# Optimization experiments

Hardware: AMD Instinct MI355X
Metric: run time of the kernel (lower is better)

The kernel has to match this reference:

```python
import jax, jax.numpy as jnp
import numpy as np

N_HEADS = 16


def setup_inputs() -> dict:
    key = jax.random.key(0)
    ks = jax.random.split(key, 9)
    B, S, D = 2, 2048, 1024
    sc = 0.02
    return {
        'x': jax.random.normal(ks[0], (B, S, D), jnp.float32),
        'Wq': jax.random.normal(ks[1], (D, D), jnp.float32) * sc,
        'bq': jax.random.normal(ks[2], (D,), jnp.float32) * sc,
        'Wk': jax.random.normal(ks[3], (D, D), jnp.float32) * sc,
        'bk': jax.random.normal(ks[4], (D,), jnp.float32) * sc,
        'Wv': jax.random.normal(ks[5], (D, D), jnp.float32) * sc,
        'bv': jax.random.normal(ks[6], (D,), jnp.float32) * sc,
        'Wo': jax.random.normal(ks[7], (D, D), jnp.float32) * sc,
        'bo': jax.random.normal(ks[8], (D,), jnp.float32) * sc,
    }


def reference(x, Wq, bq, Wk, bk, Wv, bv, Wo, bo):
    # Chunked causal prefill. The chunk-wise mask (q_pos >= kv_pos over the
    # growing KV cache) is mathematically identical to full causal attention,
    # so we compute it as one vectorized masked softmax attention.
    B, S, D = x.shape
    H = N_HEADS
    hd = D // H

    def proj(W, b):
        # torch Linear: y = x @ W.T + b ; then split heads -> [B,H,S,hd]
        y = jnp.einsum('bsd,ed->bse', x, W) + b
        return y.reshape(B, S, H, hd).transpose(0, 2, 1, 3)

    q = proj(Wq, bq)
    k = proj(Wk, bk)
    v = proj(Wv, bv)

    scores = jnp.einsum('bhqd,bhkd->bhqk', q, k) / jnp.sqrt(jnp.asarray(hd, x.dtype))
    causal = jnp.tril(jnp.ones((S, S), dtype=bool))  # [S,S]
    scores = jnp.where(causal[None, None], scores, jnp.asarray(-jnp.inf, scores.dtype))
    attn = jax.nn.softmax(scores, axis=-1)
    ctx = jnp.einsum('bhqk,bhkd->bhqd', attn, v)  # [B,H,S,hd]
    ctx = ctx.transpose(0, 2, 1, 3).reshape(B, S, D)
    out = jnp.einsum('bsd,ed->bse', ctx, Wo) + bo
    return out
```

## Files before the change

kernel.cpp:

```cpp
#include <hip/hip_runtime.h>
#include <cstdint>
#include <math.h>

typedef _Float16 f16;
typedef _Float16 f16x2 __attribute__((ext_vector_type(2)));
typedef _Float16 f16x4 __attribute__((ext_vector_type(4)));
typedef _Float16 f16x8 __attribute__((ext_vector_type(8)));
typedef __fp16   h16x2 __attribute__((ext_vector_type(2)));
typedef float    f32x4 __attribute__((ext_vector_type(4)));

__device__ __forceinline__ f32x4 mfma16(f16x8 a, f16x8 b, f32x4 c) {
  return __builtin_amdgcn_mfma_f32_16x16x32_f16(a, b, c, 0, 0, 0);
}
__device__ __forceinline__ void gl2lds16(const f16* g, f16* l) {
  __builtin_amdgcn_global_load_lds((__attribute__((address_space(1))) void*)(g),
                                   (__attribute__((address_space(3))) void*)(l),
                                   16, 0, 0);
}
__device__ __forceinline__ float fexp2(float x) { return __builtin_amdgcn_exp2f(x); }
__device__ __forceinline__ f16x2 pkrtz(float a, float b) {
  h16x2 r = __builtin_amdgcn_cvt_pkrtz(a, b);
  return __builtin_bit_cast(f16x2, r);
}
__device__ __forceinline__ float dot2acc(f16x2 a, f16x2 b, float c) {
#if __has_builtin(__builtin_amdgcn_fdot2)
  return __builtin_amdgcn_fdot2(__builtin_bit_cast(h16x2, a),
                                __builtin_bit_cast(h16x2, b), c, false);
#else
  return c + (float)a[0] * (float)b[0] + (float)a[1] * (float)b[1];
#endif
}

__global__ __launch_bounds__(256) void cvt_kernel(
    const float* __restrict__ x,  const float* __restrict__ wq, const float* __restrict__ wk,
    const float* __restrict__ wv, const float* __restrict__ wo,
    f16* __restrict__ xh, f16* __restrict__ wqkvh, f16* __restrict__ woh)
{
  const int seg = blockIdx.y;
  const float* src; f16* dst; int n;
  if      (seg == 0) { src = x;  dst = xh;              n = 4194304; }
  else if (seg == 1) { src = wq; dst = wqkvh;           n = 1048576; }
  else if (seg == 2) { src = wk; dst = wqkvh + 1048576; n = 1048576; }
  else if (seg == 3) { src = wv; dst = wqkvh + 2097152; n = 1048576; }
  else               { src = wo; dst = woh;             n = 1048576; }
  const int idx = (int)(blockIdx.x * 256 + threadIdx.x) * 8;
  if (idx >= n) return;
  f32x4 a = *(const f32x4*)(src + idx);
  f32x4 b = *(const f32x4*)(src + idx + 4);
  f16x8 h;
  h[0] = (f16)a[0]; h[1] = (f16)a[1]; h[2] = (f16)a[2]; h[3] = (f16)a[3];
  h[4] = (f16)b[0]; h[5] = (f16)b[1]; h[6] = (f16)b[2]; h[7] = (f16)b[3];
  *(f16x8*)(dst + idx) = h;
}

__global__ __launch_bounds__(256) void gemm_qkv(
    const f16* __restrict__ A, const f16* __restrict__ B,
    const float* __restrict__ bias0, const float* __restrict__ bias1, const float* __restrict__ bias2,
    f16* __restrict__ Qp, f16* __restrict__ Kp, f16* __restrict__ Vtp)
{
  constexpr int K = 1024;
  __shared__ __align__(16) f16 As[128 * 32];
  __shared__ __align__(16) f16 Bs[128 * 32];
  const int tid  = threadIdx.x;
  const int wave = tid >> 6, lane = tid & 63;
  const int quad = lane >> 4, col = lane & 15;
  const int tile_m = blockIdx.y * 128, tile_n = blockIdx.x * 128;
  const int mb = (wave >> 1) * 64, nb = (wave & 1) * 64;
  const int srow = lane >> 2, scol = (lane & 3) * 8;
  const f16* gA = A + (size_t)(tile_m + wave * 32 + srow) * K + scol;
  const f16* gB = B + (size_t)(tile_n + wave * 32 + srow) * K + scol;
  f16* lA = As + wave * 1024;
  f16* lB = Bs + wave * 1024;

  f32x4 acc[4][4] = {};
  for (int k0 = 0; k0 < K; k0 += 32) {
    gl2lds16(gA + k0,          lA);
    gl2lds16(gA + 16 * K + k0, lA + 512);
    gl2lds16(gB + k0,          lB);
    gl2lds16(gB + 16 * K + k0, lB + 512);
    __syncthreads();
    f16x8 af[4], bf[4];
    #pragma unroll
    for (int i = 0; i < 4; ++i)
      af[i] = *(const f16x8*)&As[(mb + i * 16 + col) * 32 + quad * 8];
    #pragma unroll
    for (int j = 0; j < 4; ++j)
      bf[j] = *(const f16x8*)&Bs[(nb + j * 16 + col) * 32 + quad * 8];
    #pragma unroll
    for (int i = 0; i < 4; ++i)
      #pragma unroll
      for (int j = 0; j < 4; ++j)
        acc[i][j] = mfma16(af[i], bf[j], acc[i][j]);
    __syncthreads();
  }

  #pragma unroll
  for (int j = 0; j < 4; ++j) {
    const int gn = tile_n + nb + j * 16 + col;
    const int which = gn >> 10;
    const int d = gn & 1023;
    const int h = d >> 6, hi = d & 63;
    if (which == 2) {
      const float bvv = bias2[d];
      #pragma unroll
      for (int i = 0; i < 4; ++i) {
        const int gm0 = tile_m + mb + i * 16 + quad * 4;
        const int bb = gm0 >> 11, s = gm0 & 2047;
        f16x4 pw;
        #pragma unroll
        for (int r = 0; r < 4; ++r) pw[r] = (f16)(acc[i][j][r] + bvv);
        *(f16x4*)&Vtp[(((size_t)bb * 16 + h) * 64 + hi) * 2048 + s] = pw;
      }
    } else {
      const float* bp = (which == 0) ? bias0 : bias1;
      f16* dst        = (which == 0) ? Qp    : Kp;
      const float bvv = bp[d];
      const float qs  = (which == 0) ? 0.18033688f : 1.0f;
      #pragma unroll
      for (int i = 0; i < 4; ++i) {
        #pragma unroll
        for (int r = 0; r < 4; ++r) {
          const int gm = tile_m + mb + i * 16 + quad * 4 + r;
          const int bb = gm >> 11, s = gm & 2047;
          dst[(((size_t)bb * 16 + h) * 2048 + s) * 64 + hi] = (f16)((acc[i][j][r] + bvv) * qs);
        }
      }
    }
  }
}

__global__ __launch_bounds__(128) void attn_kernel(
    const f16* __restrict__ Q, const f16* __restrict__ K, const f16* __restrict__ Vt,
    f16* __restrict__ ctx)
{
  __shared__ __align__(16) f16 Ks[64 * 72];
  __shared__ __align__(16) f16 Vts[64 * 72];
  __shared__ __align__(16) f16 Ps[2][32 * 72];
  __shared__ __align__(16) float abuf[2][32];
  __shared__ __align__(16) float lbuf[2][32];

  const int bh  = blockIdx.x;
  const int by  = blockIdx.y;
  const int qt  = (by < 16) ? by : 47 - by;
  const int tid = threadIdx.x;
  const int wave = tid >> 6, lane = tid & 63;
  const int quad = lane >> 4, col = lane & 15;
  const int b = bh >> 4, h = bh & 15;
  const size_t base = (size_t)bh * 2048 * 64;
  const size_t vtb  = (size_t)bh * 64 * 2048;

  int srow[4], sc8[4];
  #pragma unroll
  for (int i = 0; i < 4; ++i) {
    const int flat = tid + i * 128;
    srow[i] = flat >> 3;
    sc8[i]  = (flat & 7) * 8;
  }

  const int q0 = qt * 64;
  const int qa = q0 + wave * 16;
  const int qb = q0 + 32 + wave * 16;
  const f16x8 bqa0 = *(const f16x8*)&Q[base + (size_t)(qa + col) * 64 + quad * 8];
  const f16x8 bqa1 = *(const f16x8*)&Q[base + (size_t)(qa + col) * 64 + 32 + quad * 8];
  const f16x8 bqb0 = *(const f16x8*)&Q[base + (size_t)(qb + col) * 64 + quad * 8];
  const f16x8 bqb1 = *(const f16x8*)&Q[base + (size_t)(qb + col) * 64 + 32 + quad * 8];

  f32x4 cta[4] = {}, ctb[4] = {};
  float ma = -INFINITY, la = 0.f, mb = -INFINITY, lb = 0.f;

  f16x8 kr[4], vr[4];
  auto gload = [&](int t) {
    #pragma unroll
    for (int i = 0; i < 4; ++i) {
      kr[i] = *(const f16x8*)&K[base + (size_t)(t * 64 + srow[i]) * 64 + sc8[i]];
      vr[i] = *(const f16x8*)&Vt[vtb + (size_t)srow[i] * 2048 + t * 64 + sc8[i]];
    }
  };
  gload(0);

  const int nIter = qt + 1;
  for (int t = 0; t < nIter; ++t) {
    __syncthreads();
    #pragma unroll
    for (int i = 0; i < 4; ++i) {
      *(f16x8*)&Ks[srow[i] * 72 + sc8[i]]  = kr[i];
      *(f16x8*)&Vts[srow[i] * 72 + sc8[i]] = vr[i];
    }
    __syncthreads();
    if (t + 1 < nIter) gload(t + 1);

    f32x4 sa[4], sb[4];
    #pragma unroll
    for (int jt = 0; jt < 4; ++jt) {
      const int kro = (jt * 16 + col) * 72;
      const f16x8 ak0 = *(const f16x8*)&Ks[kro + quad * 8];
      const f16x8 ak1 = *(const f16x8*)&Ks[kro + 32 + quad * 8];
      f32x4 za = {}, zb = {};
      za = mfma16(ak0, bqa0, za); sa[jt] = mfma16(ak1, bqa1, za);
      zb = mfma16(ak0, bqb0, zb); sb[jt] = mfma16(ak1, bqb1, zb);
    }

    if (t == qt) {
      #pragma unroll
      for (int jt = 0; jt < 4; ++jt) {
        const int kg = t * 64 + jt * 16 + quad * 4;
        #pragma unroll
        for (int r = 0; r < 4; ++r) {
          if (kg + r > qa + col) sa[jt][r] = -1e30f;
          if (kg + r > qb + col) sb[jt][r] = -1e30f;
        }
      }
    }

    const f16x2 one2 = {(_Float16)1.f, (_Float16)1.f};
    {
      float tm = fmaxf(fmaxf(sa[0][0], sa[0][1]), fmaxf(sa[0][2], sa[0][3]));
      #pragma unroll
      for (int jt = 1; jt < 4; ++jt)
        tm = fmaxf(tm, fmaxf(fmaxf(sa[jt][0], sa[jt][1]), fmaxf(sa[jt][2], sa[jt][3])));
      tm = fmaxf(tm, __shfl_xor(tm, 16));
      tm = fmaxf(tm, __shfl_xor(tm, 32));
      const float mnew = fmaxf(ma, tm);
      const float alpha = fexp2(ma - mnew);
      ma = mnew;
      float rs = 0.f;
      #pragma unroll
      for (int jt = 0; jt < 4; ++jt) {
        const f16x2 a01 = pkrtz(fexp2(sa[jt][0] - mnew), fexp2(sa[jt][1] - mnew));
        const f16x2 a23 = pkrtz(fexp2(sa[jt][2] - mnew), fexp2(sa[jt][3] - mnew));
        rs = dot2acc(a01, one2, rs);
        rs = dot2acc(a23, one2, rs);
        f16x4 pw; pw[0] = a01[0]; pw[1] = a01[1]; pw[2] = a23[0]; pw[3] = a23[1];
        *(f16x4*)&Ps[wave][col * 72 + jt * 16 + quad * 4] = pw;
      }
      rs += __shfl_xor(rs, 16);
      rs += __shfl_xor(rs, 32);
      la = la * alpha + rs;
      if (quad == 0) abuf[wave][col] = alpha;
    }
    {
      float tm = fmaxf(fmaxf(sb[0][0], sb[0][1]), fmaxf(sb[0][2], sb[0][3]));
      #pragma unroll
      for (int jt = 1; jt < 4; ++jt)
        tm = fmaxf(tm, fmaxf(fmaxf(sb[jt][0], sb[jt][1]), fmaxf(sb[jt][2], sb[jt][3])));
      tm = fmaxf(tm, __shfl_xor(tm, 16));
      tm = fmaxf(tm, __shfl_xor(tm, 32));
      const float mnew = fmaxf(mb, tm);
      const float alpha = fexp2(mb - mnew);
      mb = mnew;
      float rs = 0.f;
      #pragma unroll
      for (int jt = 0; jt < 4; ++jt) {
        const f16x2 a01 = pkrtz(fexp2(sb[jt][0] - mnew), fexp2(sb[jt][1] - mnew));
        const f16x2 a23 = pkrtz(fexp2(sb[jt][2] - mnew), fexp2(sb[jt][3] - mnew));
        rs = dot2acc(a01, one2, rs);
        rs = dot2acc(a23, one2, rs);
        f16x4 pw; pw[0] = a01[0]; pw[1] = a01[1]; pw[2] = a23[0]; pw[3] = a23[1];
        *(f16x4*)&Ps[wave][(16 + col) * 72 + jt * 16 + quad * 4] = pw;
      }
      rs += __shfl_xor(rs, 16);
      rs += __shfl_xor(rs, 32);
      lb = lb * alpha + rs;
      if (quad == 0) abuf[wave][16 + col] = alpha;
    }

    __asm__ volatile("s_waitcnt lgkmcnt(0)" ::: "memory");
    const f32x4 ava = *(const f32x4*)&abuf[wave][quad * 4];
    const f32x4 avb = *(const f32x4*)&abuf[wave][16 + quad * 4];
    #pragma unroll
    for (int jd = 0; jd < 4; ++jd) { cta[jd] *= ava; ctb[jd] *= avb; }

    const f16x8 apa0 = *(const f16x8*)&Ps[wave][col * 72 + quad * 8];
    const f16x8 apa1 = *(const f16x8*)&Ps[wave][col * 72 + 32 + quad * 8];
    const f16x8 apb0 = *(const f16x8*)&Ps[wave][(16 + col) * 72 + quad * 8];
    const f16x8 apb1 = *(const f16x8*)&Ps[wave][(16 + col) * 72 + 32 + quad * 8];
    #pragma unroll
    for (int jd = 0; jd < 4; ++jd) {
      const int vro = (jd * 16 + col) * 72;
      const f16x8 bv0 = *(const f16x8*)&Vts[vro + quad * 8];
      const f16x8 bv1 = *(const f16x8*)&Vts[vro + 32 + quad * 8];
      cta[jd] = mfma16(apa1, bv1, mfma16(apa0, bv0, cta[jd]));
      ctb[jd] = mfma16(apb1, bv1, mfma16(apb0, bv0, ctb[jd]));
    }
  }

  if (quad == 0) { lbuf[wave][col] = la; lbuf[wave][16 + col] = lb; }
  __asm__ volatile("s_waitcnt lgkmcnt(0)" ::: "memory");
  const f32x4 lva = *(const f32x4*)&lbuf[wave][quad * 4];
  const f32x4 lvb = *(const f32x4*)&lbuf[wave][16 + quad * 4];
  #pragma unroll
  for (int jd = 0; jd < 4; ++jd) {
    #pragma unroll
    for (int r = 0; r < 4; ++r) {
      const int qga = qa + quad * 4 + r;
      const int qgb = qb + quad * 4 + r;
      const int d = h * 64 + jd * 16 + col;
      ctx[((size_t)b * 2048 + qga) * 1024 + d] = (f16)(cta[jd][r] / lva[r]);
      ctx[((size_t)b * 2048 + qgb) * 1024 + d] = (f16)(ctb[jd][r] / lvb[r]);
    }
  }
}

__global__ __launch_bounds__(256) void gemm_o(
    const f16* __restrict__ A, const f16* __restrict__ B, const float* __restrict__ bias,
    float* __restrict__ Out)
{
  constexpr int K = 1024;
  __shared__ __align__(16) f16 As[128 * 32];
  __shared__ __align__(16) f16 Bs[64 * 32];
  const int tid  = threadIdx.x;
  const int wave = tid >> 6, lane = tid & 63;
  const int quad = lane >> 4, col = lane & 15;
  const int tile_m = blockIdx.y * 128, tile_n = blockIdx.x * 64;
  const int mb = wave * 32;
  const int srow = lane >> 2, scol = (lane & 3) * 8;
  const f16* gA = A + (size_t)(tile_m + wave * 32 + srow) * K + scol;
  const f16* gB = B + (size_t)(tile_n + wave * 16 + srow) * K + scol;
  f16* lA = As + wave * 1024;
  f16* lB = Bs + wave * 512;

  f32x4 acc[2][4] = {};
  for (int k0 = 0; k0 < K; k0 += 32) {
    gl2lds16(gA + k0,          lA);
    gl2lds16(gA + 16 * K + k0, lA + 512);
    gl2lds16(gB + k0,          lB);
    __syncthreads();
    f16x8 af[2], bf[4];
    #pragma unroll
    for (int i = 0; i < 2; ++i)
      af[i] = *(const f16x8*)&As[(mb + i * 16 + col) * 32 + quad * 8];
    #pragma unroll
    for (int j = 0; j < 4; ++j)
      bf[j] = *(const f16x8*)&Bs[(j * 16 + col) * 32 + quad * 8];
    #pragma unroll
    for (int i = 0; i < 2; ++i)
      #pragma unroll
      for (int j = 0; j < 4; ++j)
        acc[i][j] = mfma16(af[i], bf[j], acc[i][j]);
    __syncthreads();
  }

  #pragma unroll
  for (int j = 0; j < 4; ++j) {
    const int gn = tile_n + j * 16 + col;
    const float bvv = bias[gn];
    #pragma unroll
    for (int i = 0; i < 2; ++i) {
      #pragma unroll
      for (int r = 0; r < 4; ++r) {
        const int gm = tile_m + mb + i * 16 + quad * 4 + r;
        Out[(size_t)gm * 1024 + gn] = acc[i][j][r] + bvv;
      }
    }
  }
}

extern "C" void kernel_launch(void* const* d_in, const int* in_sizes, int n_in,
                              void* d_out, int out_size, void* d_ws, size_t ws_size,
                              hipStream_t stream)
{
  const float* x  = (const float*)d_in[0];
  const float* Wq = (const float*)d_in[1];
  const float* bq = (const float*)d_in[2];
  const float* Wk = (const float*)d_in[3];
  const float* bk = (const float*)d_in[4];
  const float* Wv = (const float*)d_in[5];
  const float* bv = (const float*)d_in[6];
  const float* Wo = (const float*)d_in[7];
  const float* bo = (const float*)d_in[8];
  float* out = (float*)d_out;

  f16* ws = (f16*)d_ws;
  const size_t M1 = 1048576;
  f16* xh    = ws;
  f16* wqkvh = ws + 4  * M1;
  f16* woh   = ws + 7  * M1;
  f16* Qh    = ws + 8  * M1;
  f16* Kh    = ws + 12 * M1;
  f16* Vth   = ws + 16 * M1;
  f16* ctxh  = ws + 20 * M1;

  cvt_kernel<<<dim3(2048, 5), 256, 0, stream>>>(x, Wq, Wk, Wv, Wo, xh, wqkvh, woh);
  gemm_qkv<<<dim3(24, 32), 256, 0, stream>>>(xh, wqkvh, bq, bk, bv, Qh, Kh, Vth);
  attn_kernel<<<dim3(32, 32), 128, 0, stream>>>(Qh, Kh, Vth, ctxh);
  gemm_o<<<dim3(16, 32), 256, 0, stream>>>(ctxh, woh, bo, out);
}
```

Baseline: 214.2 us.

## Restructure attention to single-wave blocks loading K/V straight from global memory

The attention kernel now runs one 64-thread wave per block, each handling 32 query rows, on a 32x64 grid scheduled longest-causal-work first. K and V^T fragments are read directly from global memory into registers, which removes the LDS staging buffers and both __syncthreads per tile. The alpha and row-sum broadcasts move from LDS to lane shuffles. In exchange, K/V tiles are no longer shared between waves, so L2 traffic doubles, and global loads are no longer prefetched a tile ahead, which exposes load latency unless occupancy hides it.

```diff
diff --git a/kernel.cpp b/kernel.cpp
--- a/kernel.cpp
+++ b/kernel.cpp
@@ -129,37 +129,23 @@
   }
 }
 
-__global__ __launch_bounds__(128) void attn_kernel(
+__global__ __launch_bounds__(64, 2) void attn_kernel(
     const f16* __restrict__ Q, const f16* __restrict__ K, const f16* __restrict__ Vt,
     f16* __restrict__ ctx)
 {
-  __shared__ __align__(16) f16 Ks[64 * 72];
-  __shared__ __align__(16) f16 Vts[64 * 72];
-  __shared__ __align__(16) f16 Ps[2][32 * 72];
-  __shared__ __align__(16) float abuf[2][32];
-  __shared__ __align__(16) float lbuf[2][32];
-
-  const int bh  = blockIdx.x;
-  const int by  = blockIdx.y;
-  const int qt  = (by < 16) ? by : 47 - by;
-  const int tid = threadIdx.x;
-  const int wave = tid >> 6, lane = tid & 63;
+  __shared__ __align__(16) f16 Ps[32 * 72];
+
+  const int bh   = blockIdx.x;
+  const int slot = 63 - (int)blockIdx.y;
+  const int lane = threadIdx.x;
   const int quad = lane >> 4, col = lane & 15;
   const int b = bh >> 4, h = bh & 15;
   const size_t base = (size_t)bh * 2048 * 64;
   const size_t vtb  = (size_t)bh * 64 * 2048;
 
-  int srow[4], sc8[4];
-  #pragma unroll
-  for (int i = 0; i < 4; ++i) {
-    const int flat = tid + i * 128;
-    srow[i] = flat >> 3;
-    sc8[i]  = (flat & 7) * 8;
-  }
-
-  const int q0 = qt * 64;
-  const int qa = q0 + wave * 16;
-  const int qb = q0 + 32 + wave * 16;
+  const int q0 = slot * 32;
+  const int qa = q0, qb = q0 + 16;
+
   const f16x8 bqa0 = *(const f16x8*)&Q[base + (size_t)(qa + col) * 64 + quad * 8];
   const f16x8 bqa1 = *(const f16x8*)&Q[base + (size_t)(qa + col) * 64 + 32 + quad * 8];
   const f16x8 bqb0 = *(const f16x8*)&Q[base + (size_t)(qb + col) * 64 + quad * 8];
@@ -168,39 +154,34 @@
   f32x4 cta[4] = {}, ctb[4] = {};
   float ma = -INFINITY, la = 0.f, mb = -INFINITY, lb = 0.f;
 
-  f16x8 kr[4], vr[4];
-  auto gload = [&](int t) {
-    #pragma unroll
-    for (int i = 0; i < 4; ++i) {
-      kr[i] = *(const f16x8*)&K[base + (size_t)(t * 64 + srow[i]) * 64 + sc8[i]];
-      vr[i] = *(const f16x8*)&Vt[vtb + (size_t)srow[i] * 2048 + t * 64 + sc8[i]];
-    }
-  };
-  gload(0);
-
-  const int nIter = qt + 1;
+  const f16* kf = K  + base + (size_t)col * 64 + quad * 8;
+  const f16* vf = Vt + vtb  + (size_t)col * 2048 + quad * 8;
+
+  const int nIter = (slot >> 1) + 1;
   for (int t = 0; t < nIter; ++t) {
-    __syncthreads();
-    #pragma unroll
-    for (int i = 0; i < 4; ++i) {
-      *(f16x8*)&Ks[srow[i] * 72 + sc8[i]]  = kr[i];
-      *(f16x8*)&Vts[srow[i] * 72 + sc8[i]] = vr[i];
-    }
-    __syncthreads();
-    if (t + 1 < nIter) gload(t + 1);
+    f16x8 ak0[4], ak1[4], bv0[4], bv1[4];
+    const f16* kt = kf + (size_t)t * 4096;
+    const f16* vt = vf + t * 64;
+    #pragma unroll
+    for (int j = 0; j < 4; ++j) {
+      ak0[j] = *(const f16x8*)&kt[(size_t)j * 1024];
+      ak1[j] = *(const f16x8*)&kt[(size_t)j * 1024 + 32];
+    }
+    #pragma unroll
+    for (int j = 0; j < 4; ++j) {
+      bv0[j] = *(const f16x8*)&vt[(size_t)j * 32768];
+      bv1[j] = *(const f16x8*)&vt[(size_t)j * 32768 + 32];
+    }
 
     f32x4 sa[4], sb[4];
     #pragma unroll
     for (int jt = 0; jt < 4; ++jt) {
-      const int kro = (jt * 16 + col) * 72;
-      const f16x8 ak0 = *(const f16x8*)&Ks[kro + quad * 8];
-      const f16x8 ak1 = *(const f16x8*)&Ks[kro + 32 + quad * 8];
       f32x4 za = {}, zb = {};
-      za = mfma16(ak0, bqa0, za); sa[jt] = mfma16(ak1, bqa1, za);
-      zb = mfma16(ak0, bqb0, zb); sb[jt] = mfma16(ak1, bqb1, zb);
-    }
-
-    if (t == qt) {
+      za = mfma16(ak0[jt], bqa0, za); sa[jt] = mfma16(ak1[jt], bqa1, za);
+      zb = mfma16(ak0[jt], bqb0, zb); sb[jt] = mfma16(ak1[jt], bqb1, zb);
+    }
+
+    if (t == nIter - 1) {
       #pragma unroll
       for (int jt = 0; jt < 4; ++jt) {
         const int kg = t * 64 + jt * 16 + quad * 4;
@@ -213,6 +194,7 @@
     }
 
     const f16x2 one2 = {(_Float16)1.f, (_Float16)1.f};
+    f32x4 ava, avb;
     {
       float tm = fmaxf(fmaxf(sa[0][0], sa[0][1]), fmaxf(sa[0][2], sa[0][3]));
       #pragma unroll
@@ -231,12 +213,13 @@
         rs = dot2acc(a01, one2, rs);
         rs = dot2acc(a23, one2, rs);
         f16x4 pw; pw[0] = a01[0]; pw[1] = a01[1]; pw[2] = a23[0]; pw[3] = a23[1];
-        *(f16x4*)&Ps[wave][col * 72 + jt * 16 + quad * 4] = pw;
+        *(f16x4*)&Ps[col * 72 + jt * 16 + quad * 4] = pw;
       }
       rs += __shfl_xor(rs, 16);
       rs += __shfl_xor(rs, 32);
       la = la * alpha + rs;
-      if (quad == 0) abuf[wave][col] = alpha;
+      #pragma unroll
+      for (int r = 0; r < 4; ++r) ava[r] = __shfl(alpha, quad * 4 + r);
     }
     {
       float tm = fmaxf(fmaxf(sb[0][0], sb[0][1]), fmaxf(sb[0][2], sb[0][3]));
@@ -256,38 +239,37 @@
         rs = dot2acc(a01, one2, rs);
         rs = dot2acc(a23, one2, rs);
         f16x4 pw; pw[0] = a01[0]; pw[1] = a01[1]; pw[2] = a23[0]; pw[3] = a23[1];
-        *(f16x4*)&Ps[wave][(16 + col) * 72 + jt * 16 + quad * 4] = pw;
+        *(f16x4*)&Ps[(16 + col) * 72 + jt * 16 + quad * 4] = pw;
       }
       rs += __shfl_xor(rs, 16);
       rs += __shfl_xor(rs, 32);
       lb = lb * alpha + rs;
-      if (quad == 0) abuf[wave][16 + col] = alpha;
-    }
+      #pragma unroll
+      for (int r = 0; r < 4; ++r) avb[r] = __shfl(alpha, quad * 4 + r);
+    }
+
+    #pragma unroll
+    for (int jd = 0; jd < 4; ++jd) { cta[jd] *= ava; ctb[jd] *= avb; }
 
     __asm__ volatile("s_waitcnt lgkmcnt(0)" ::: "memory");
-    const f32x4 ava = *(const f32x4*)&abuf[wave][quad * 4];
-    const f32x4 avb = *(const f32x4*)&abuf[wave][16 + quad * 4];
-    #pragma unroll
-    for (int jd = 0; jd < 4; ++jd) { cta[jd] *= ava; ctb[jd] *= avb; }
-
-    const f16x8 apa0 = *(const f16x8*)&Ps[wave][col * 72 + quad * 8];
-    const f16x8 apa1 = *(const f16x8*)&Ps[wave][col * 72 + 32 + quad * 8];
-    const f16x8 apb0 = *(const f16x8*)&Ps[wave][(16 + col) * 72 + quad * 8];
-    const f16x8 apb1 = *(const f16x8*)&Ps[wave][(16 + col) * 72 + 32 + quad * 8];
+
+    const f16x8 apa0 = *(const f16x8*)&Ps[col * 72 + quad * 8];
+    const f16x8 apa1 = *(const f16x8*)&Ps[col * 72 + 32 + quad * 8];
+    const f16x8 apb0 = *(const f16x8*)&Ps[(16 + col) * 72 + quad * 8];
+    const f16x8 apb1 = *(const f16x8*)&Ps[(16 + col) * 72 + 32 + quad * 8];
     #pragma unroll
     for (int jd = 0; jd < 4; ++jd) {
-      const int vro = (jd * 16 + col) * 72;
-      const f16x8 bv0 = *(const f16x8*)&Vts[vro + quad * 8];
-      const f16x8 bv1 = *(const f16x8*)&Vts[vro + 32 + quad * 8];
-      cta[jd] = mfma16(apa1, bv1, mfma16(apa0, bv0, cta[jd]));
-      ctb[jd] = mfma16(apb1, bv1, mfma16(apb0, bv0, ctb[jd]));
-    }
-  }
-
-  if (quad == 0) { lbuf[wave][col] = la; lbuf[wave][16 + col] = lb; }
-  __asm__ volatile("s_waitcnt lgkmcnt(0)" ::: "memory");
-  const f32x4 lva = *(const f32x4*)&lbuf[wave][quad * 4];
-  const f32x4 lvb = *(const f32x4*)&lbuf[wave][16 + quad * 4];
+      cta[jd] = mfma16(apa1, bv1[jd], mfma16(apa0, bv0[jd], cta[jd]));
+      ctb[jd] = mfma16(apb1, bv1[jd], mfma16(apb0, bv0[jd], ctb[jd]));
+    }
+  }
+
+  f32x4 lva, lvb;
+  #pragma unroll
+  for (int r = 0; r < 4; ++r) {
+    lva[r] = __shfl(la, quad * 4 + r);
+    lvb[r] = __shfl(lb, quad * 4 + r);
+  }
   #pragma unroll
   for (int jd = 0; jd < 4; ++jd) {
     #pragma unroll
@@ -382,6 +364,6 @@
 
   cvt_kernel<<<dim3(2048, 5), 256, 0, stream>>>(x, Wq, Wk, Wv, Wo, xh, wqkvh, woh);
   gemm_qkv<<<dim3(24, 32), 256, 0, stream>>>(xh, wqkvh, bq, bk, bv, Qh, Kh, Vth);
-  attn_kernel<<<dim3(32, 32), 128, 0, stream>>>(Qh, Kh, Vth, ctxh);
+  attn_kernel<<<dim3(32, 64), 64, 0, stream>>>(Qh, Kh, Vth, ctxh);
   gemm_o<<<dim3(16, 32), 256, 0, stream>>>(ctxh, woh, bo, out);
 }
```

Result: slower. 229.8 us (+7.3%).
